# Kernel tuning notes

Measured on AMD Instinct MI355X. Metric: run time of the kernel, lower is better.

## Reference

```python
import jax, jax.numpy as jnp
import numpy as np

DIM = 512
CHUNK = 64
LN_EPS = 1e-5


def setup_inputs() -> dict:
    key = jax.random.key(0)
    ks = jax.random.split(key, 9)
    B, S, D = 4, 4096, DIM
    x = jax.random.normal(ks[0], (B, S, D), dtype=jnp.float32)
    # Linear weights stored as [in, out] (equivalent to torch W.T)
    W_omega = jax.random.normal(ks[1], (D, D), dtype=jnp.float32) / np.sqrt(D)
    b_omega = jnp.zeros((D,), dtype=jnp.float32)
    log_scale = jnp.full((D,), np.log(0.1), dtype=jnp.float32)
    ln_gamma = jnp.ones((4 * D,), dtype=jnp.float32)
    ln_beta = jnp.zeros((4 * D,), dtype=jnp.float32)
    W1 = jax.random.normal(ks[2], (4 * D, 2 * D), dtype=jnp.float32) / np.sqrt(4 * D)
    b1 = jnp.zeros((2 * D,), dtype=jnp.float32)
    W2 = jax.random.normal(ks[3], (2 * D, D), dtype=jnp.float32) / np.sqrt(2 * D)
    b2 = jnp.zeros((D,), dtype=jnp.float32)
    return {"x": x, "W_omega": W_omega, "b_omega": b_omega, "log_scale": log_scale,
            "ln_gamma": ln_gamma, "ln_beta": ln_beta, "W1": W1, "b1": b1, "W2": W2, "b2": b2}


def reference(x, W_omega, b_omega, log_scale, ln_gamma, ln_beta, W1, b1, W2, b2):
    B, S, D = x.shape
    C = CHUNK
    # S chosen as multiple of C, so pad_len == 0 (matches torch no-pad branch)
    N = S // C
    omega = x @ W_omega + b_omega                      # [B,S,D]
    oc = omega.reshape(B, N, C, D)
    xc = x.reshape(B, N, C, D)
    pos = jnp.arange(1, C + 1, dtype=x.dtype)          # [C]
    pos_scale = (1.0 / jnp.sqrt(pos))[None, None, :, None]
    scale = jnp.exp(log_scale)
    phi = jnp.cumsum(oc * scale * pos_scale, axis=2)   # [B,N,C,D]
    cos_phi = jnp.cos(phi)
    sin_phi = jnp.sin(phi)
    cr = xc * cos_phi                                   # content modulated real
    ci = xc * sin_phi                                   # content modulated imag
    pos_norm = pos[None, None, :, None]
    mr = jnp.cumsum(cr, axis=2) / pos_norm              # memory real
    mi = jnp.cumsum(ci, axis=2) / pos_norm              # memory imag
    rr = mr * cos_phi + mi * sin_phi                    # retrieved real
    ri = mi * cos_phi - mr * sin_phi                    # retrieved imag
    ctx = jnp.concatenate([cr.reshape(B, S, D), ci.reshape(B, S, D),
                           rr.reshape(B, S, D), ri.reshape(B, S, D)], axis=-1)  # [B,S,4D]
    mu = jnp.mean(ctx, axis=-1, keepdims=True)
    var = jnp.mean((ctx - mu) ** 2, axis=-1, keepdims=True)
    h = (ctx - mu) / jnp.sqrt(var + LN_EPS) * ln_gamma + ln_beta
    h = h @ W1 + b1
    h = jax.nn.gelu(h, approximate=False)               # torch GELU default = exact erf
    out = h @ W2 + b2                                   # dropout is identity at eval
    return x + out
```

## Files before the change

### kernel.cpp

```cpp
#include <hip/hip_runtime.h>
#include <hip/hip_bf16.h>
#include <math.h>


typedef __bf16 bf16x8 __attribute__((ext_vector_type(8)));
typedef __bf16 bf16x4 __attribute__((ext_vector_type(4)));
typedef __bf16 bf16x2 __attribute__((ext_vector_type(2)));
typedef float  f32x4  __attribute__((ext_vector_type(4)));

typedef __attribute__((address_space(1))) void* gas_ptr;
typedef __attribute__((address_space(3))) void* las_ptr;

__device__ __forceinline__ void load_lds16(const void* g, void* l) {
    __builtin_amdgcn_global_load_lds((gas_ptr)g, (las_ptr)l, 16, 0, 0);
}

__device__ __forceinline__ void transpose_tile(const float* __restrict__ in,
                                               __bf16* __restrict__ out,
                                               int K, int N, int bx, int by,
                                               float (*tile)[33])
{
    const int tid = threadIdx.x;
    const int tx = tid & 31, ty = tid >> 5;
    const int n0 = bx * 32, k0 = by * 32;
    #pragma unroll
    for (int i = 0; i < 32; i += 8)
        tile[ty + i][tx] = in[(size_t)(k0 + ty + i) * N + n0 + tx];
    __syncthreads();
    #pragma unroll
    for (int i = 0; i < 32; i += 8)
        out[(size_t)(n0 + ty + i) * K + k0 + tx] = (__bf16)tile[tx][ty + i];
}

__global__ __launch_bounds__(256)
void prep_kernel(const float* __restrict__ x, __bf16* __restrict__ xb,
                 const float* __restrict__ W_omega, __bf16* __restrict__ womT,
                 const float* __restrict__ W1, __bf16* __restrict__ w1T,
                 const float* __restrict__ W2, __bf16* __restrict__ w2T)
{
    __shared__ float tile[32][33];
    const int bid = blockIdx.x;
    if (bid < 8192) {
        int i = bid * 256 + threadIdx.x;
        float4 v = ((const float4*)x)[i];
        bf16x4 o = { (__bf16)v.x, (__bf16)v.y, (__bf16)v.z, (__bf16)v.w };
        ((bf16x4*)xb)[i] = o;
    } else if (bid < 8448) {
        int t = bid - 8192;
        transpose_tile(W_omega, womT, 512, 512, t & 15, t >> 4, tile);
    } else if (bid < 10496) {
        int t = bid - 8448;
        transpose_tile(W1, w1T, 2048, 1024, t & 31, t >> 5, tile);
    } else {
        int t = bid - 10496;
        transpose_tile(W2, w2T, 1024, 512, t & 15, t >> 4, tile);
    }
}

template<int MODE>
__global__ __launch_bounds__(256)
void gemm_kernel(const __bf16* __restrict__ A, const __bf16* __restrict__ Bt,
                 const float* __restrict__ bias, const __bf16* __restrict__ resid,
                 void* __restrict__ out, int M, int N, int K)
{
    __shared__ __bf16 As[2][128 * 64];
    __shared__ __bf16 Bs[2][128 * 64];

    const int tid     = threadIdx.x;
    const int tiles_n = N >> 7;
    const int ln_tn   = __ffs(tiles_n) - 1;
    const int per_m   = (M >> 7) >> 3;

    const int xcd = blockIdx.x & 7;
    const int j   = blockIdx.x >> 3;
    const int tile_m = (xcd * per_m + (j >> ln_tn)) << 7;
    const int tile_n = (j & (tiles_n - 1)) << 7;

    const int wave = tid >> 6;
    const int lane = tid & 63;

    const int srow = lane >> 3;
    const int scol = ((lane & 7) ^ srow) << 3;

    const __bf16* Ags = A  + (size_t)(tile_m + wave * 32 + srow) * K + scol;
    const __bf16* Bgs = Bt + (size_t)(tile_n + wave * 32 + srow) * K + scol;

    const int m0 = (wave >> 1) << 6;
    const int n0 = (wave & 1) << 6;
    const int lr = lane & 15;
    const int q  = lane >> 4;
    const int l7 = lane & 7;
    const int fc0 = ((0 + q) ^ l7) << 3;
    const int fc1 = ((4 + q) ^ l7) << 3;

    f32x4 acc[4][4];
    #pragma unroll
    for (int i = 0; i < 4; ++i)
        #pragma unroll
        for (int jj = 0; jj < 4; ++jj)
            acc[i][jj] = (f32x4){0.f, 0.f, 0.f, 0.f};

    const int nIter = K >> 6;

    #pragma unroll
    for (int c = 0; c < 4; ++c) {
        load_lds16(Ags + (size_t)(c * 8) * K, &As[0][(wave * 32 + c * 8) * 64]);
        load_lds16(Bgs + (size_t)(c * 8) * K, &Bs[0][(wave * 32 + c * 8) * 64]);
    }

    for (int it = 0; it < nIter; ++it) {
        const int cur = it & 1;
        __syncthreads();
        if (it + 1 < nIter) {
            const int nk = (it + 1) << 6;
            #pragma unroll
            for (int c = 0; c < 4; ++c) {
                load_lds16(Ags + nk + (size_t)(c * 8) * K, &As[cur ^ 1][(wave * 32 + c * 8) * 64]);
                load_lds16(Bgs + nk + (size_t)(c * 8) * K, &Bs[cur ^ 1][(wave * 32 + c * 8) * 64]);
            }
        }

        const __bf16* as = As[cur];
        const __bf16* bs = Bs[cur];
        {
            bf16x8 af[4], bq[4];
            #pragma unroll
            for (int i = 0; i < 4; ++i)
                af[i] = *(const bf16x8*)&as[(m0 + i * 16 + lr) * 64 + fc0];
            #pragma unroll
            for (int jj = 0; jj < 4; ++jj)
                bq[jj] = *(const bf16x8*)&bs[(n0 + jj * 16 + lr) * 64 + fc0];
            #pragma unroll
            for (int i = 0; i < 4; ++i)
                #pragma unroll
                for (int jj = 0; jj < 4; ++jj)
                    acc[i][jj] = __builtin_amdgcn_mfma_f32_16x16x32_bf16(af[i], bq[jj], acc[i][jj], 0, 0, 0);
        }
        {
            bf16x8 af[4], bq[4];
            #pragma unroll
            for (int i = 0; i < 4; ++i)
                af[i] = *(const bf16x8*)&as[(m0 + i * 16 + lr) * 64 + fc1];
            #pragma unroll
            for (int jj = 0; jj < 4; ++jj)
                bq[jj] = *(const bf16x8*)&bs[(n0 + jj * 16 + lr) * 64 + fc1];
            #pragma unroll
            for (int i = 0; i < 4; ++i)
                #pragma unroll
                for (int jj = 0; jj < 4; ++jj)
                    acc[i][jj] = __builtin_amdgcn_mfma_f32_16x16x32_bf16(af[i], bq[jj], acc[i][jj], 0, 0, 0);
        }
    }

    const int orow0 = tile_m + m0 + (q << 2);
    const int ocol0 = tile_n + n0 + lr;
    #pragma unroll
    for (int i = 0; i < 4; ++i) {
        #pragma unroll
        for (int jj = 0; jj < 4; ++jj) {
            const int col = ocol0 + jj * 16;
            const float bv = bias[col];
            #pragma unroll
            for (int r = 0; r < 4; ++r) {
                const int row = orow0 + i * 16 + r;
                float v = acc[i][jj][r] + bv;
                size_t idx = (size_t)row * N + col;
                if (MODE == 0) {
                    ((__bf16*)out)[idx] = (__bf16)v;
                } else if (MODE == 1) {
                    float g = 0.5f * v * (1.0f + erff(v * 0.70710678118654752f));
                    ((__bf16*)out)[idx] = (__bf16)g;
                } else {
                    ((float*)out)[idx] = v + (float)resid[idx];
                }
            }
        }
    }
}

template<int MODE>
__global__ __launch_bounds__(512, 2)
void gemm256_kernel(const __bf16* __restrict__ A, const __bf16* __restrict__ Bt,
                    const float* __restrict__ bias, void* __restrict__ out,
                    int M, int N, int K)
{
    __shared__ __bf16 As[4][256 * 32];
    __shared__ __bf16 Bs[4][256 * 32];

    const int tid  = threadIdx.x;
    const int wv   = tid >> 6;
    const int lane = tid & 63;
    const int wm   = wv >> 2;
    const int wn   = wv & 3;

    const int tiles_n = N >> 8;
    const int ln_tn   = __ffs(tiles_n) - 1;
    const int per_m   = (M >> 8) >> 3;

    const int xcd = blockIdx.x & 7;
    const int j   = blockIdx.x >> 3;
    const int tile_m = (xcd * per_m + (j >> ln_tn)) << 8;
    const int tile_n = (j & (tiles_n - 1)) << 8;

    const int srow = 16 * wv + (lane >> 2);
    const int sig8 = (((lane & 3) ^ ((lane >> 3) & 3)) << 3);

    const __bf16* Ag = A  + (size_t)(tile_m + srow) * K + sig8;
    const __bf16* Bg = Bt + (size_t)(tile_n + srow) * K + sig8;
    const size_t rowK128 = (size_t)128 * K;
    const int lbase = wv * 512;

    const int lr    = lane & 15;
    const int q4    = lane >> 4;
    const int fslot = ((q4 ^ ((lane >> 1) & 3)) << 3);
    const int arow0 = wm * 128 + lr;
    const int brow0 = wn * 64 + lr;

    f32x4 acc[8][4];
    #pragma unroll
    for (int i = 0; i < 8; ++i)
        #pragma unroll
        for (int jj = 0; jj < 4; ++jj)
            acc[i][jj] = (f32x4){0.f, 0.f, 0.f, 0.f};

    const int NKS = K >> 5;

    auto stage = [&](int ks) {
        const int slot = ks & 3;
        const __bf16* ag = Ag + (ks << 5);
        const __bf16* bg = Bg + (ks << 5);
        load_lds16(ag,           &As[slot][lbase]);
        load_lds16(ag + rowK128, &As[slot][4096 + lbase]);
        load_lds16(bg,           &Bs[slot][lbase]);
        load_lds16(bg + rowK128, &Bs[slot][4096 + lbase]);
    };

    if (0 < NKS) stage(0);
    if (1 < NKS) stage(1);
    if (2 < NKS) stage(2);

    for (int ks = 0; ks < NKS; ++ks) {
        if (ks + 2 < NKS)      asm volatile("s_waitcnt vmcnt(8)" ::: "memory");
        else if (ks + 1 < NKS) asm volatile("s_waitcnt vmcnt(4)" ::: "memory");
        else                   asm volatile("s_waitcnt vmcnt(0)" ::: "memory");
        __builtin_amdgcn_s_barrier();
        asm volatile("" ::: "memory");

        if (ks + 3 < NKS) stage(ks + 3);

        const __bf16* as = As[ks & 3];
        const __bf16* bs = Bs[ks & 3];
        bf16x8 af[8], bq[4];
        #pragma unroll
        for (int i = 0; i < 8; ++i)
            af[i] = *(const bf16x8*)&as[(arow0 + i * 16) * 32 + fslot];
        #pragma unroll
        for (int jj = 0; jj < 4; ++jj)
            bq[jj] = *(const bf16x8*)&bs[(brow0 + jj * 16) * 32 + fslot];

        __builtin_amdgcn_s_setprio(1);
        #pragma unroll
        for (int i = 0; i < 8; ++i)
            #pragma unroll
            for (int jj = 0; jj < 4; ++jj)
                acc[i][jj] = __builtin_amdgcn_mfma_f32_16x16x32_bf16(af[i], bq[jj], acc[i][jj], 0, 0, 0);
        __builtin_amdgcn_s_setprio(0);
    }

    const int orow0 = tile_m + wm * 128 + (q4 << 2);
    const int ocol0 = tile_n + wn * 64 + lr;
    #pragma unroll
    for (int i = 0; i < 8; ++i) {
        #pragma unroll
        for (int jj = 0; jj < 4; ++jj) {
            const int col = ocol0 + jj * 16;
            const float bv = bias[col];
            #pragma unroll
            for (int r = 0; r < 4; ++r) {
                const int row = orow0 + i * 16 + r;
                float v = acc[i][jj][r] + bv;
                if (MODE == 1) {
                    float g = 0.5f * v * (1.0f + erff(v * 0.70710678118654752f));
                    ((__bf16*)out)[(size_t)row * N + col] = (__bf16)g;
                } else {
                    ((__bf16*)out)[(size_t)row * N + col] = (__bf16)v;
                }
            }
        }
    }
}

__global__ __launch_bounds__(512)
void scan_ln_kernel(const __bf16* __restrict__ xb, const __bf16* __restrict__ omega,
                    const float* __restrict__ log_scale,
                    const float* __restrict__ gamma, const float* __restrict__ beta,
                    __bf16* __restrict__ ctx)
{
    const int chunk = blockIdx.x;
    const int d     = threadIdx.x;
    const int lane  = d & 63, wv = d >> 6;
    const size_t base = (size_t)chunk * 64 * 512;

    const float scale = expf(log_scale[d]);
    const float g0 = gamma[d], g1 = gamma[512 + d], g2 = gamma[1024 + d], g3 = gamma[1536 + d];
    const float e0 = beta[d],  e1 = beta[512 + d],  e2 = beta[1024 + d],  e3 = beta[1536 + d];

    float phi = 0.f, scr = 0.f, sci = 0.f;
    __shared__ float red[2][16];

    float om_n = (float)omega[base + d];
    float xv_n = (float)xb[base + d];

    for (int c = 0; c < 64; ++c) {
        const float om = om_n;
        const float xv = xv_n;
        if (c < 63) {
            om_n = (float)omega[base + (size_t)(c + 1) * 512 + d];
            xv_n = (float)xb[base + (size_t)(c + 1) * 512 + d];
        }
        phi += om * scale * rsqrtf((float)(c + 1));
        float sp, cp;
        __sincosf(phi, &sp, &cp);
        const float cr = xv * cp, ci = xv * sp;
        scr += cr; sci += ci;
        const float inv = 1.0f / (float)(c + 1);
        const float mr = scr * inv, mi = sci * inv;
        const float rr = mr * cp + mi * sp;
        const float ri = mi * cp - mr * sp;

        float s  = cr + ci + rr + ri;
        float s2 = cr * cr + ci * ci + rr * rr + ri * ri;
        #pragma unroll
        for (int o = 32; o > 0; o >>= 1) {
            s  += __shfl_down(s, o);
            s2 += __shfl_down(s2, o);
        }
        if (lane == 0) { red[c & 1][wv] = s; red[c & 1][8 + wv] = s2; }
        __syncthreads();
        float S = 0.f, S2 = 0.f;
        #pragma unroll
        for (int i = 0; i < 8; ++i) { S += red[c & 1][i]; S2 += red[c & 1][8 + i]; }
        const float mu   = S * (1.0f / 2048.0f);
        const float var  = S2 * (1.0f / 2048.0f) - mu * mu;
        const float rstd = rsqrtf(var + 1e-5f);

        const size_t ob = ((size_t)chunk * 64 + c) * 2048;
        ctx[ob + d]        = (__bf16)(((cr - mu) * rstd) * g0 + e0);
        ctx[ob + 512 + d]  = (__bf16)(((ci - mu) * rstd) * g1 + e1);
        ctx[ob + 1024 + d] = (__bf16)(((rr - mu) * rstd) * g2 + e2);
        ctx[ob + 1536 + d] = (__bf16)(((ri - mu) * rstd) * g3 + e3);
    }
}

extern "C" void kernel_launch(void* const* d_in, const int* in_sizes, int n_in,
                              void* d_out, int out_size, void* d_ws, size_t ws_size,
                              hipStream_t stream)
{
    const float* x         = (const float*)d_in[0];
    const float* W_omega   = (const float*)d_in[1];
    const float* b_omega   = (const float*)d_in[2];
    const float* log_scale = (const float*)d_in[3];
    const float* ln_gamma  = (const float*)d_in[4];
    const float* ln_beta   = (const float*)d_in[5];
    const float* W1        = (const float*)d_in[6];
    const float* b1        = (const float*)d_in[7];
    const float* W2        = (const float*)d_in[8];
    const float* b2        = (const float*)d_in[9];
    float* out = (float*)d_out;

    char* ws = (char*)d_ws;
    __bf16* xb    = (__bf16*)(ws);
    __bf16* womT  = (__bf16*)(ws + 16777216);
    __bf16* w1T   = (__bf16*)(ws + 17301504);
    __bf16* w2T   = (__bf16*)(ws + 21495808);
    __bf16* omega = (__bf16*)(ws + 22544384);
    __bf16* hbuf  = (__bf16*)(ws + 22544384);
    __bf16* ctx   = (__bf16*)(ws + 56098816);

    prep_kernel<<<11008, 256, 0, stream>>>(x, xb, W_omega, womT, W1, w1T, W2, w2T);

    gemm_kernel<0><<<512, 256, 0, stream>>>(xb, womT, b_omega, nullptr, omega, 16384, 512, 512);

    scan_ln_kernel<<<256, 512, 0, stream>>>(xb, omega, log_scale, ln_gamma, ln_beta, ctx);

    gemm256_kernel<1><<<256, 512, 0, stream>>>(ctx, w1T, b1, hbuf, 16384, 1024, 2048);

    gemm_kernel<2><<<512, 256, 0, stream>>>(hbuf, w2T, b2, xb, out, 16384, 512, 1024);
}
```

Baseline: 285.1 us.

## Double-buffer LDS fragment reads in registers to overlap with MFMA in GEMM

Restructures the 256x256 GEMM main loop so the LDS fragments for the next K-step are loaded into a second register set while the MFMAs for the current step run. The loop is unrolled by two to ping-pong between the two register sets, and the global-to-LDS prefetch distance grows from three stages to four. Launch bounds drop from 2 to 1 blocks per CU to make room for the extra registers; the 128KB of LDS per block likely already limited occupancy to one block. The loop now assumes the K-step count is even, which holds for the K sizes here.

```diff
diff --git a/kernel.cpp b/kernel.cpp
--- a/kernel.cpp
+++ b/kernel.cpp
@@ -179,7 +179,7 @@
 }
 
 template<int MODE>
-__global__ __launch_bounds__(512, 2)
+__global__ __launch_bounds__(512, 1)
 void gemm256_kernel(const __bf16* __restrict__ A, const __bf16* __restrict__ Bt,
                     const float* __restrict__ bias, void* __restrict__ out,
                     int M, int N, int K)
@@ -235,37 +235,57 @@
         load_lds16(bg + rowK128, &Bs[slot][4096 + lbase]);
     };
 
-    if (0 < NKS) stage(0);
-    if (1 < NKS) stage(1);
-    if (2 < NKS) stage(2);
-
-    for (int ks = 0; ks < NKS; ++ks) {
-        if (ks + 2 < NKS)      asm volatile("s_waitcnt vmcnt(8)" ::: "memory");
-        else if (ks + 1 < NKS) asm volatile("s_waitcnt vmcnt(4)" ::: "memory");
-        else                   asm volatile("s_waitcnt vmcnt(0)" ::: "memory");
-        __builtin_amdgcn_s_barrier();
-        asm volatile("" ::: "memory");
-
-        if (ks + 3 < NKS) stage(ks + 3);
-
-        const __bf16* as = As[ks & 3];
-        const __bf16* bs = Bs[ks & 3];
-        bf16x8 af[8], bq[4];
-        #pragma unroll
-        for (int i = 0; i < 8; ++i)
-            af[i] = *(const bf16x8*)&as[(arow0 + i * 16) * 32 + fslot];
-        #pragma unroll
-        for (int jj = 0; jj < 4; ++jj)
-            bq[jj] = *(const bf16x8*)&bs[(brow0 + jj * 16) * 32 + fslot];
-
-        __builtin_amdgcn_s_setprio(1);
-        #pragma unroll
-        for (int i = 0; i < 8; ++i)
-            #pragma unroll
-            for (int jj = 0; jj < 4; ++jj)
-                acc[i][jj] = __builtin_amdgcn_mfma_f32_16x16x32_bf16(af[i], bq[jj], acc[i][jj], 0, 0, 0);
-        __builtin_amdgcn_s_setprio(0);
-    }
+    bf16x8 afA[8], bqA[4], afB[8], bqB[4];
+
+#define G256_READ(KS, NAF, NBQ)                                               \
+    {                                                                         \
+        const __bf16* as_ = As[(KS) & 3];                                     \
+        const __bf16* bs_ = Bs[(KS) & 3];                                     \
+        _Pragma("unroll")                                                     \
+        for (int i_ = 0; i_ < 8; ++i_)                                        \
+            NAF[i_] = *(const bf16x8*)&as_[(arow0 + i_ * 16) * 32 + fslot];   \
+        _Pragma("unroll")                                                     \
+        for (int j_ = 0; j_ < 4; ++j_)                                        \
+            NBQ[j_] = *(const bf16x8*)&bs_[(brow0 + j_ * 16) * 32 + fslot];   \
+    }
+
+#define G256_PHASE(KS, CAF, CBQ, NAF, NBQ)                                    \
+    {                                                                         \
+        const int ks_ = (KS);                                                 \
+        const int r_  = NKS - 1 - ks_;                                        \
+        if (r_ >= 3)      asm volatile("s_waitcnt vmcnt(8)" ::: "memory");    \
+        else if (r_ == 2) asm volatile("s_waitcnt vmcnt(4)" ::: "memory");    \
+        else if (r_ == 1) asm volatile("s_waitcnt vmcnt(0)" ::: "memory");    \
+        __builtin_amdgcn_s_barrier();                                         \
+        asm volatile("" ::: "memory");                                        \
+        if (ks_ + 4 < NKS) stage(ks_ + 4);                                    \
+        if (ks_ + 1 < NKS) G256_READ(ks_ + 1, NAF, NBQ)                       \
+        __builtin_amdgcn_s_setprio(1);                                        \
+        _Pragma("unroll")                                                     \
+        for (int i_ = 0; i_ < 8; ++i_)                                        \
+            _Pragma("unroll")                                                 \
+            for (int j_ = 0; j_ < 4; ++j_)                                    \
+                acc[i_][j_] = __builtin_amdgcn_mfma_f32_16x16x32_bf16(        \
+                    CAF[i_], CBQ[j_], acc[i_][j_], 0, 0, 0);                  \
+        __builtin_amdgcn_s_setprio(0);                                        \
+        asm volatile("s_waitcnt lgkmcnt(0)" ::: "memory");                    \
+    }
+
+    stage(0); stage(1); stage(2);
+    asm volatile("s_waitcnt vmcnt(8)" ::: "memory");
+    __builtin_amdgcn_s_barrier();
+    asm volatile("" ::: "memory");
+    stage(3);
+    G256_READ(0, afA, bqA)
+    asm volatile("s_waitcnt lgkmcnt(0)" ::: "memory");
+
+    for (int ks = 0; ks < NKS; ks += 2) {
+        G256_PHASE(ks,     afA, bqA, afB, bqB)
+        G256_PHASE(ks + 1, afB, bqB, afA, bqA)
+    }
+
+#undef G256_PHASE
+#undef G256_READ
 
     const int orow0 = tile_m + wm * 128 + (q4 << 2);
     const int ocol0 = tile_n + wn * 64 + lr;
```

Result: no change. 285.7 us (+0.2%).
